# Optimization experiments

Hardware: AMD Instinct MI355X
Metric: run time of the kernel (lower is better)

Reference implementation:

```python
import jax, jax.numpy as jnp
import numpy as np
import math

B, T, D = 2, 2048, 1024
H, HS = 16, 64  # n_heads, head_size; D == H*HS


def setup_inputs() -> dict:
    key = jax.random.key(0)
    k1, k2, k3 = jax.random.split(key, 3)
    x = jax.random.normal(k1, (B, T, D), dtype=jnp.float32)
    w_qkv = jax.random.normal(k2, (D, 3 * D), dtype=jnp.float32) * (1.0 / math.sqrt(D))
    b_qkv = jnp.zeros((3 * D,), dtype=jnp.float32)
    w_out = jax.random.normal(k3, (D, D), dtype=jnp.float32) * (1.0 / math.sqrt(D))
    b_out = jnp.zeros((D,), dtype=jnp.float32)
    return {"x": x, "w_qkv": w_qkv, "b_qkv": b_qkv, "w_out": w_out, "b_out": b_out}


def reference(x, w_qkv, b_qkv, w_out, b_out):
    b, t, d = x.shape
    qkv = x @ w_qkv + b_qkv                       # (B,T,3D)
    q, k, v = jnp.split(qkv, 3, axis=-1)
    # (B,T,D) -> (B,H,T,HS)
    q = q.reshape(b, t, H, HS).transpose(0, 2, 1, 3)
    k = k.reshape(b, t, H, HS).transpose(0, 2, 1, 3)
    v = v.reshape(b, t, H, HS).transpose(0, 2, 1, 3)
    scale = 1.0 / math.sqrt(HS)
    attn = jnp.einsum('bhqd,bhkd->bhqk', q, k) * scale  # (B,H,T,T)
    causal = jnp.tril(jnp.ones((t, t), dtype=bool))
    attn = jnp.where(causal[None, None], attn, -jnp.inf)
    attn = jax.nn.softmax(attn, axis=-1)
    o = jnp.einsum('bhqk,bhkd->bhqd', attn, v)          # (B,H,T,HS)
    o = o.transpose(0, 2, 1, 3).reshape(b, t, d)
    return o @ w_out + b_out
```

## Files before the change

### kernel.cpp

```cpp
#include <hip/hip_runtime.h>
#include <math.h>

#define B_  2
#define T_  2048
#define D_  1024
#define H_  16
#define HS_ 64
#define M_  (B_*T_)

typedef __bf16 bf16x8 __attribute__((ext_vector_type(8)));
typedef float  f32x4  __attribute__((ext_vector_type(4)));
typedef unsigned short u16;

static __device__ __forceinline__ u16 f2bf(float f) {
    __bf16 h = (__bf16)f;
    return *reinterpret_cast<u16*>(&h);
}

static __device__ __forceinline__ void glds16(const u16* g, u16* l) {
    __builtin_amdgcn_global_load_lds(
        (const __attribute__((address_space(1))) void*)g,
        (__attribute__((address_space(3))) void*)l, 16, 0, 0);
}

__global__ __launch_bounds__(256) void prep_kernel(
    const float* __restrict__ x, const float* __restrict__ w_qkv,
    const float* __restrict__ w_out,
    u16* __restrict__ Xb, u16* __restrict__ WqkvT, u16* __restrict__ WoutT)
{
    int bid = blockIdx.x;
    if (bid < 4096) {
        int i = (bid * 256 + threadIdx.x) * 4;
        float4 v = *reinterpret_cast<const float4*>(x + i);
        ushort4 o;
        o.x = f2bf(v.x); o.y = f2bf(v.y); o.z = f2bf(v.z); o.w = f2bf(v.w);
        *reinterpret_cast<ushort4*>(Xb + i) = o;
        return;
    }
    const float* in; u16* out; int C; int c0, r0;
    if (bid < 4096 + 3072) {
        int t = bid - 4096;
        in = w_qkv; out = WqkvT; C = 3 * D_;
        c0 = (t % 96) * 32; r0 = (t / 96) * 32;
    } else {
        int t = bid - 7168;
        in = w_out; out = WoutT; C = D_;
        c0 = (t & 31) * 32; r0 = (t >> 5) * 32;
    }
    __shared__ float tile[32][33];
    int tr = threadIdx.x >> 3, tc4 = (threadIdx.x & 7) * 4;
    float4 v = *reinterpret_cast<const float4*>(in + (size_t)(r0 + tr) * C + c0 + tc4);
    tile[tr][tc4+0] = v.x; tile[tr][tc4+1] = v.y;
    tile[tr][tc4+2] = v.z; tile[tr][tc4+3] = v.w;
    __syncthreads();
    ushort4 o;
    o.x = f2bf(tile[tc4+0][tr]); o.y = f2bf(tile[tc4+1][tr]);
    o.z = f2bf(tile[tc4+2][tr]); o.w = f2bf(tile[tc4+3][tr]);
    *reinterpret_cast<ushort4*>(out + (size_t)(c0 + tr) * D_ + r0 + tc4) = o;
}

__global__ __launch_bounds__(512, 2) void gemm_qkv(
    const u16* __restrict__ A, const u16* __restrict__ Bt,
    const float* __restrict__ bias,
    u16* __restrict__ Qb, u16* __restrict__ Kb, u16* __restrict__ Vt)
{
    constexpr int K  = D_;
    constexpr int NT = K / 64;

    __shared__ u16 LDS[2][2][2][8192];

    const int tid  = threadIdx.x;
    const int lane = tid & 63, wave = tid >> 6;
    const int wm = wave >> 2, wn = wave & 3;
    const int quad = lane >> 4, lr = lane & 15;
    const int bm = blockIdx.x, bn = blockIdx.y;

    const u16* Ab = A  + (size_t)(bm * 256) * K;
    const u16* Bb = Bt + (size_t)(bn * 256) * K;

    const int r0 = tid >> 2;
    const int c0 = (tid & 3) ^ ((tid >> 3) & 3);
    const u16* sA0 = Ab + (size_t)r0 * K + c0 * 8;
    const u16* sA1 = sA0 + (size_t)128 * K;
    const u16* sB0 = Bb + (size_t)r0 * K + c0 * 8;
    const u16* sB1 = sB0 + (size_t)128 * K;
    const int d0 = tid * 8, d1 = (tid + 512) * 8;

    const int swz = (lr >> 1) & 3;
    const int eA = ((wm*128 + lr) * 4 + (quad ^ swz)) * 8;
    const int eB = ((wn*64  + lr) * 4 + (quad ^ swz)) * 8;

    f32x4 acc[8][4] = {};

#define STG(mat, kh, tt) do { \
        u16* _d = &LDS[(tt) & 1][mat][kh][0]; \
        const int _ko = (tt) * 64 + (kh) * 32; \
        glds16(((mat) ? sB0 : sA0) + _ko, _d + d0); \
        glds16(((mat) ? sB1 : sA1) + _ko, _d + d1); \
    } while (0)

#define MFMA_QUAD(mh) do { \
        __builtin_amdgcn_s_setprio(1); \
        _Pragma("unroll") \
        for (int i_ = 0; i_ < 4; ++i_) \
            _Pragma("unroll") \
            for (int j_ = 0; j_ < 4; ++j_) \
                acc[(mh)*4 + i_][j_] = __builtin_amdgcn_mfma_f32_16x16x32_bf16( \
                    a[i_], b[j_], acc[(mh)*4 + i_][j_], 0, 0, 0); \
        __builtin_amdgcn_s_setprio(0); \
    } while (0)

    STG(0,0,0); STG(1,0,0); STG(0,1,0); STG(1,1,0);
    asm volatile("s_waitcnt vmcnt(4)" ::: "memory");
    __builtin_amdgcn_s_barrier();

    for (int t = 0; t < NT; ++t) {
        const int cb = t & 1;
        const bool last = (t == NT - 1);
        const u16* Ar0 = &LDS[cb][0][0][0];
        const u16* Ar1 = &LDS[cb][0][1][0];
        const u16* Br0 = &LDS[cb][1][0][0];
        const u16* Br1 = &LDS[cb][1][1][0];
        bf16x8 a[4], b[4];

        #pragma unroll
        for (int i = 0; i < 4; ++i) a[i] = *reinterpret_cast<const bf16x8*>(Ar0 + eA + i*512);
        #pragma unroll
        for (int j = 0; j < 4; ++j) b[j] = *reinterpret_cast<const bf16x8*>(Br0 + eB + j*512);
        if (!last) STG(0,0,t+1);
        __builtin_amdgcn_s_barrier();
        asm volatile("s_waitcnt lgkmcnt(0)" ::: "memory");
        MFMA_QUAD(0);
        __builtin_amdgcn_s_barrier();

        #pragma unroll
        for (int i = 0; i < 4; ++i) a[i] = *reinterpret_cast<const bf16x8*>(Ar0 + eA + (i+4)*512);
        if (!last) STG(1,0,t+1);
        __builtin_amdgcn_s_barrier();
        asm volatile("s_waitcnt lgkmcnt(0)" ::: "memory");
        MFMA_QUAD(1);
        if (!last) { asm volatile("s_waitcnt vmcnt(4)" ::: "memory"); }
        else       { asm volatile("s_waitcnt vmcnt(0)" ::: "memory"); }
        __builtin_amdgcn_s_barrier();

        #pragma unroll
        for (int i = 0; i < 4; ++i) a[i] = *reinterpret_cast<const bf16x8*>(Ar1 + eA + i*512);
        #pragma unroll
        for (int j = 0; j < 4; ++j) b[j] = *reinterpret_cast<const bf16x8*>(Br1 + eB + j*512);
        if (!last) STG(0,1,t+1);
        __builtin_amdgcn_s_barrier();
        asm volatile("s_waitcnt lgkmcnt(0)" ::: "memory");
        MFMA_QUAD(0);
        __builtin_amdgcn_s_barrier();

        #pragma unroll
        for (int i = 0; i < 4; ++i) a[i] = *reinterpret_cast<const bf16x8*>(Ar1 + eA + (i+4)*512);
        if (!last) STG(1,1,t+1);
        __builtin_amdgcn_s_barrier();
        asm volatile("s_waitcnt lgkmcnt(0)" ::: "memory");
        MFMA_QUAD(1);
        asm volatile("s_waitcnt vmcnt(4)" ::: "memory");
        __builtin_amdgcn_s_barrier();
    }
#undef STG
#undef MFMA_QUAD

    #pragma unroll
    for (int i = 0; i < 8; ++i) {
        int m0 = bm*256 + wm*128 + i*16 + quad*4;
        #pragma unroll
        for (int j = 0; j < 4; ++j) {
            int ncol = bn*256 + wn*64 + j*16 + lr;
            float bv = bias[ncol];
            float v4[4];
            #pragma unroll
            for (int r = 0; r < 4; ++r) v4[r] = acc[i][j][r] + bv;
            int bb = m0 >> 11, t0 = m0 & (T_ - 1);
            int s = ncol >> 10, rem = ncol & 1023;
            int h = rem >> 6, d = rem & 63;
            int bh = bb * H_ + h;
            if (s == 0) {
                #pragma unroll
                for (int r = 0; r < 4; ++r)
                    Qb[((size_t)bh*T_ + t0 + r)*HS_ + d] = f2bf(v4[r] * 0.1803368801111244f);
            } else if (s == 1) {
                #pragma unroll
                for (int r = 0; r < 4; ++r)
                    Kb[((size_t)bh*T_ + t0 + r)*HS_ + d] = f2bf(v4[r]);
            } else {
                ushort4 o;
                o.x = f2bf(v4[0]); o.y = f2bf(v4[1]);
                o.z = f2bf(v4[2]); o.w = f2bf(v4[3]);
                *reinterpret_cast<ushort4*>(&Vt[((size_t)bh*HS_ + d)*T_ + t0]) = o;
            }
        }
    }
}

template<int MODE, int BM, int BN, int WM, int WN, int NTH>
__global__ __launch_bounds__(NTH, 2) void gemm_bt2(
    const u16* __restrict__ A, const u16* __restrict__ Bt,
    const float* __restrict__ bias,
    float* __restrict__ Cf,
    int M, int N, int K)
{
    constexpr int MF  = BM / WM / 16;
    constexpr int NF  = BN / WN / 16;
    constexpr int NLA = BM * 8 / NTH;
    constexpr int NLB = BN * 8 / NTH;

    __shared__ u16 As[2][BM * 64];
    __shared__ u16 Bs[2][BN * 64];

    const int tid  = threadIdx.x;
    const int lane = tid & 63, wave = tid >> 6;
    const int wm = wave / WN, wn = wave % WN;
    const int quad = lane >> 4, lr = lane & 15, x7 = lane & 7;
    const int bm = blockIdx.x, bn = blockIdx.y;

    const u16* Ab = A  + (size_t)(bm * BM) * K;
    const u16* Bb = Bt + (size_t)(bn * BN) * K;

    const u16* srcA[NLA]; int dA[NLA];
    const u16* srcB[NLB]; int dB[NLB];
    #pragma unroll
    for (int j = 0; j < NLA; ++j) {
        int ci = j * NTH + tid, r = ci >> 3, c = (ci & 7) ^ (r & 7);
        srcA[j] = Ab + (size_t)r * K + c * 8;
        dA[j] = ci * 8;
    }
    #pragma unroll
    for (int j = 0; j < NLB; ++j) {
        int ci = j * NTH + tid, r = ci >> 3, c = (ci & 7) ^ (r & 7);
        srcB[j] = Bb + (size_t)r * K + c * 8;
        dB[j] = ci * 8;
    }

    const int eA0 = (wm*(BM/WM) + lr)*64 + ((quad    ) ^ x7)*8;
    const int eA1 = (wm*(BM/WM) + lr)*64 + ((quad | 4) ^ x7)*8;
    const int eB0 = (wn*(BN/WN) + lr)*64 + ((quad    ) ^ x7)*8;
    const int eB1 = (wn*(BN/WN) + lr)*64 + ((quad | 4) ^ x7)*8;

    f32x4 acc[MF][NF] = {};
    const int NT = K >> 6;

    #pragma unroll
    for (int j = 0; j < NLA; ++j) glds16(srcA[j], &As[0][dA[j]]);
    #pragma unroll
    for (int j = 0; j < NLB; ++j) glds16(srcB[j], &Bs[0][dB[j]]);
    #pragma unroll
    for (int j = 0; j < NLA; ++j) glds16(srcA[j] + 64, &As[1][dA[j]]);
    #pragma unroll
    for (int j = 0; j < NLB; ++j) glds16(srcB[j] + 64, &Bs[1][dB[j]]);
    asm volatile("s_waitcnt vmcnt(8)" ::: "memory");
    __builtin_amdgcn_s_barrier();

    for (int t = 0; t < NT; ++t) {
        const u16* Ac = As[t & 1];
        const u16* Bc = Bs[t & 1];
        bf16x8 a[MF], b[NF];

        #pragma unroll
        for (int i = 0; i < MF; ++i)
            a[i] = *reinterpret_cast<const bf16x8*>(Ac + eA0 + i*1024);
        #pragma unroll
        for (int j = 0; j < NF; ++j)
            b[j] = *reinterpret_cast<const bf16x8*>(Bc + eB0 + j*1024);
        __builtin_amdgcn_s_setprio(1);
        #pragma unroll
        for (int i = 0; i < MF; ++i)
            #pragma unroll
            for (int j = 0; j < NF; ++j)
                acc[i][j] = __builtin_amdgcn_mfma_f32_16x16x32_bf16(a[i], b[j], acc[i][j], 0, 0, 0);
        __builtin_amdgcn_s_setprio(0);

        #pragma unroll
        for (int i = 0; i < MF; ++i)
            a[i] = *reinterpret_cast<const bf16x8*>(Ac + eA1 + i*1024);
        #pragma unroll
        for (int j = 0; j < NF; ++j)
            b[j] = *reinterpret_cast<const bf16x8*>(Bc + eB1 + j*1024);
        asm volatile("s_waitcnt lgkmcnt(0)" ::: "memory");
        __builtin_amdgcn_s_barrier();

        if (t + 2 < NT) {
            const int k0 = (t + 2) << 6;
            u16* Ad = As[t & 1]; u16* Bd = Bs[t & 1];
            #pragma unroll
            for (int j = 0; j < NLA; ++j) glds16(srcA[j] + k0, Ad + dA[j]);
            #pragma unroll
            for (int j = 0; j < NLB; ++j) glds16(srcB[j] + k0, Bd + dB[j]);
        }

        __builtin_amdgcn_s_setprio(1);
        #pragma unroll
        for (int i = 0; i < MF; ++i)
            #pragma unroll
            for (int j = 0; j < NF; ++j)
                acc[i][j] = __builtin_amdgcn_mfma_f32_16x16x32_bf16(a[i], b[j], acc[i][j], 0, 0, 0);
        __builtin_amdgcn_s_setprio(0);

        if (t + 2 < NT) { asm volatile("s_waitcnt vmcnt(8)" ::: "memory"); }
        else           { asm volatile("s_waitcnt vmcnt(0)" ::: "memory"); }
        __builtin_amdgcn_s_barrier();
    }

    #pragma unroll
    for (int i = 0; i < MF; ++i) {
        int m0 = bm*BM + wm*(BM/WM) + i*16 + quad*4;
        #pragma unroll
        for (int j = 0; j < NF; ++j) {
            int ncol = bn*BN + wn*(BN/WN) + j*16 + lr;
            float bv = bias[ncol];
            #pragma unroll
            for (int r = 0; r < 4; ++r)
                Cf[(size_t)(m0 + r) * N + ncol] = acc[i][j][r] + bv;
        }
    }
}

__global__ __launch_bounds__(256) void attn_kernel(
    const u16* __restrict__ Qb, const u16* __restrict__ Kb,
    const u16* __restrict__ Vt, u16* __restrict__ Ob)
{
    __shared__ u16 Ks[64 * 64];
    __shared__ u16 Vs[64 * 64];
    __shared__ u16 Ps[4][16 * 64];

    int tid  = threadIdx.x;
    int lane = tid & 63, wave = tid >> 6;
    int quad = lane >> 4, lr = lane & 15;

    int lin = blockIdx.x;
    int bh  = (lin & 7) + 8 * ((lin >> 3) & 3);
    int idx = lin >> 5;
    int qt  = idx < 16 ? idx : 47 - idx;
    int qw  = qt * 64 + wave * 16;

    const u16* Qp = Qb + ((size_t)bh * T_ + qw) * HS_;
    bf16x8 qf[2];
    #pragma unroll
    for (int h2 = 0; h2 < 2; ++h2)
        qf[h2] = *reinterpret_cast<const bf16x8*>(Qp + lr*HS_ + h2*32 + quad*8);

    f32x4 Oa[4] = {};
    float lrow[4] = {0.f, 0.f, 0.f, 0.f};

    int e      = quad ^ (lr & 7);
    int rb0    = (lr * 8 + e) * 8;
    int rb1    = (lr * 8 + (e ^ 4)) * 8;
    int offw[4][4];
    #pragma unroll
    for (int nt = 0; nt < 4; ++nt)
        #pragma unroll
        for (int r = 0; r < 4; ++r) {
            int prow = quad*4 + r;
            offw[nt][r] = (prow*8 + ((nt*2 + (lr >> 3)) ^ (prow & 7)))*8 + (lr & 7);
        }
    u16* Psw = Ps[wave];

    int srow = tid >> 3;
    int scol = ((tid & 7) ^ (srow & 7)) * 8;
    const u16* kp0 = Kb + ((size_t)bh*T_ + srow     )*HS_ + scol;
    const u16* kp1 = Kb + ((size_t)bh*T_ + srow + 32)*HS_ + scol;
    const u16* vp0 = Vt + ((size_t)bh*HS_ + srow     )*T_ + scol;
    const u16* vp1 = Vt + ((size_t)bh*HS_ + srow + 32)*T_ + scol;

    bf16x8 kpre0 = *reinterpret_cast<const bf16x8*>(kp0);
    bf16x8 kpre1 = *reinterpret_cast<const bf16x8*>(kp1);
    bf16x8 vpre0 = *reinterpret_cast<const bf16x8*>(vp0);
    bf16x8 vpre1 = *reinterpret_cast<const bf16x8*>(vp1);

    for (int jt = 0; jt <= qt; ++jt) {
        __syncthreads();
        reinterpret_cast<bf16x8*>(Ks)[tid]       = kpre0;
        reinterpret_cast<bf16x8*>(Ks)[tid + 256] = kpre1;
        reinterpret_cast<bf16x8*>(Vs)[tid]       = vpre0;
        reinterpret_cast<bf16x8*>(Vs)[tid + 256] = vpre1;
        if (jt < qt) {
            kp0 += 64*HS_; kp1 += 64*HS_; vp0 += 64; vp1 += 64;
            kpre0 = *reinterpret_cast<const bf16x8*>(kp0);
            kpre1 = *reinterpret_cast<const bf16x8*>(kp1);
            vpre0 = *reinterpret_cast<const bf16x8*>(vp0);
            vpre1 = *reinterpret_cast<const bf16x8*>(vp1);
        }
        __syncthreads();

        f32x4 Sa[4] = {};
        #pragma unroll
        for (int nt = 0; nt < 4; ++nt) {
            bf16x8 bk0 = *reinterpret_cast<const bf16x8*>(Ks + rb0 + nt*1024);
            bf16x8 bk1 = *reinterpret_cast<const bf16x8*>(Ks + rb1 + nt*1024);
            Sa[nt] = __builtin_amdgcn_mfma_f32_16x16x32_bf16(qf[0], bk0, Sa[nt], 0, 0, 0);
            Sa[nt] = __builtin_amdgcn_mfma_f32_16x16x32_bf16(qf[1], bk1, Sa[nt], 0, 0, 0);
        }

        if (jt == qt) {
            int kb = jt * 64;
            #pragma unroll
            for (int nt = 0; nt < 4; ++nt)
                #pragma unroll
                for (int r = 0; r < 4; ++r) {
                    int kg = kb + nt*16 + lr;
                    int qg = qw + quad*4 + r;
                    if (kg > qg) Sa[nt][r] = -INFINITY;
                }
        }

        #pragma unroll
        for (int nt = 0; nt < 4; ++nt)
            #pragma unroll
            for (int r = 0; r < 4; ++r) {
                float pv = __builtin_amdgcn_exp2f(Sa[nt][r]);
                lrow[r] += pv;
                Psw[offw[nt][r]] = f2bf(pv);
            }

        #pragma unroll
        for (int kk = 0; kk < 2; ++kk) {
            int rb = kk ? rb1 : rb0;
            bf16x8 pa = *reinterpret_cast<const bf16x8*>(Psw + rb);
            #pragma unroll
            for (int nt = 0; nt < 4; ++nt) {
                bf16x8 vb = *reinterpret_cast<const bf16x8*>(Vs + rb + nt*1024);
                Oa[nt] = __builtin_amdgcn_mfma_f32_16x16x32_bf16(pa, vb, Oa[nt], 0, 0, 0);
            }
        }
    }

    int b = bh >> 4, h = bh & 15;
    #pragma unroll
    for (int r = 0; r < 4; ++r) {
        float s = lrow[r];
        #pragma unroll
        for (int off = 8; off >= 1; off >>= 1)
            s += __shfl_xor(s, off, 64);
        float inv = 1.f / s;
        int qg = qw + quad*4 + r;
        #pragma unroll
        for (int nt = 0; nt < 4; ++nt) {
            int d = nt*16 + lr;
            Ob[((size_t)b*T_ + qg)*D_ + h*HS_ + d] = f2bf(Oa[nt][r] * inv);
        }
    }
}

extern "C" void kernel_launch(void* const* d_in, const int* in_sizes, int n_in,
                              void* d_out, int out_size, void* d_ws, size_t ws_size,
                              hipStream_t stream) {
    (void)in_sizes; (void)n_in; (void)out_size; (void)ws_size;
    const float* x     = (const float*)d_in[0];
    const float* w_qkv = (const float*)d_in[1];
    const float* b_qkv = (const float*)d_in[2];
    const float* w_out = (const float*)d_in[3];
    const float* b_out = (const float*)d_in[4];
    float* out = (float*)d_out;

    char* ws = (char*)d_ws;
    u16* Xb    = (u16*)ws; ws += (size_t)M_ * D_ * 2;
    u16* WqkvT = (u16*)ws; ws += (size_t)3 * D_ * D_ * 2;
    u16* WoutT = (u16*)ws; ws += (size_t)D_ * D_ * 2;
    u16* Qb    = (u16*)ws; ws += (size_t)M_ * D_ * 2;
    u16* Kb    = (u16*)ws; ws += (size_t)M_ * D_ * 2;
    u16* Vt    = (u16*)ws; ws += (size_t)M_ * D_ * 2;
    u16* Ob    = (u16*)ws; ws += (size_t)M_ * D_ * 2;

    prep_kernel<<<8192, 256, 0, stream>>>(x, w_qkv, w_out, Xb, WqkvT, WoutT);
    gemm_qkv<<<dim3(M_/256, 3*D_/256), 512, 0, stream>>>(
        Xb, WqkvT, b_qkv, Qb, Kb, Vt);
    attn_kernel<<<1024, 256, 0, stream>>>(Qb, Kb, Vt, Ob);
    gemm_bt2<1, 128, 128, 2, 2, 256><<<dim3(M_/128, D_/128), 256, 0, stream>>>(
        Ob, WoutT, b_out, out, M_, D_, D_);
}
```

Baseline: 174.1 us.

## Rewrite output GEMM with half-K-step LDS staging and finer prefetch

Replaces the templated output-projection GEMM with a specialized 128x128 kernel. Each 64-wide K tile is split into two 32-wide halves in separate LDS buffers with a new 4-way XOR swizzle, and the next tile's half is prefetched right after the current half's fragments are read. The aim is finer-grained overlap of global-to-LDS loads with MFMA work and keeping the prefetch only one tile ahead. The cost is more barriers per K step, and the shallower prefetch depth (one tile ahead instead of two) may expose more memory latency.

```diff
diff --git a/kernel.cpp b/kernel.cpp
--- a/kernel.cpp
+++ b/kernel.cpp
@@ -197,120 +197,107 @@
     }
 }
 
-template<int MODE, int BM, int BN, int WM, int WN, int NTH>
-__global__ __launch_bounds__(NTH, 2) void gemm_bt2(
+__global__ __launch_bounds__(256, 2) void gemm_out(
     const u16* __restrict__ A, const u16* __restrict__ Bt,
-    const float* __restrict__ bias,
-    float* __restrict__ Cf,
-    int M, int N, int K)
+    const float* __restrict__ bias, float* __restrict__ Cf)
 {
-    constexpr int MF  = BM / WM / 16;
-    constexpr int NF  = BN / WN / 16;
-    constexpr int NLA = BM * 8 / NTH;
-    constexpr int NLB = BN * 8 / NTH;
-
-    __shared__ u16 As[2][BM * 64];
-    __shared__ u16 Bs[2][BN * 64];
+    constexpr int K  = D_;
+    constexpr int N  = D_;
+    constexpr int NT = K / 64;
+
+    __shared__ u16 LDS[2][2][2][4096];
 
     const int tid  = threadIdx.x;
     const int lane = tid & 63, wave = tid >> 6;
-    const int wm = wave / WN, wn = wave % WN;
-    const int quad = lane >> 4, lr = lane & 15, x7 = lane & 7;
+    const int wm = wave >> 1, wn = wave & 1;
+    const int quad = lane >> 4, lr = lane & 15;
     const int bm = blockIdx.x, bn = blockIdx.y;
 
-    const u16* Ab = A  + (size_t)(bm * BM) * K;
-    const u16* Bb = Bt + (size_t)(bn * BN) * K;
-
-    const u16* srcA[NLA]; int dA[NLA];
-    const u16* srcB[NLB]; int dB[NLB];
+    const u16* Ab = A  + (size_t)(bm * 128) * K;
+    const u16* Bb = Bt + (size_t)(bn * 128) * K;
+
+    const int r0 = tid >> 2;
+    const int c0 = (tid & 3) ^ ((tid >> 3) & 3);
+    const u16* sA0 = Ab + (size_t)r0 * K + c0 * 8;
+    const u16* sA1 = sA0 + (size_t)64 * K;
+    const u16* sB0 = Bb + (size_t)r0 * K + c0 * 8;
+    const u16* sB1 = sB0 + (size_t)64 * K;
+    const int d0 = tid * 8, d1 = (tid + 256) * 8;
+
+    const int swz = (lr >> 1) & 3;
+    const int eA = ((wm*64 + lr) * 4 + (quad ^ swz)) * 8;
+    const int eB = ((wn*64 + lr) * 4 + (quad ^ swz)) * 8;
+
+    f32x4 acc[4][4] = {};
+
+#define STGO(kh, tt) do { \
+        const int _ko = (tt) * 64 + (kh) * 32; \
+        glds16(sA0 + _ko, &LDS[(tt) & 1][0][kh][0] + d0); \
+        glds16(sA1 + _ko, &LDS[(tt) & 1][0][kh][0] + d1); \
+        glds16(sB0 + _ko, &LDS[(tt) & 1][1][kh][0] + d0); \
+        glds16(sB1 + _ko, &LDS[(tt) & 1][1][kh][0] + d1); \
+    } while (0)
+
+    STGO(0, 0); STGO(1, 0);
+    asm volatile("s_waitcnt vmcnt(4)" ::: "memory");
+    __builtin_amdgcn_s_barrier();
+
+    for (int t = 0; t < NT; ++t) {
+        const int cb = t & 1;
+        const bool last = (t == NT - 1);
+        bf16x8 a[4], b[4];
+
+        {
+            const u16* Ar = &LDS[cb][0][0][0];
+            const u16* Br = &LDS[cb][1][0][0];
+            #pragma unroll
+            for (int i = 0; i < 4; ++i) a[i] = *reinterpret_cast<const bf16x8*>(Ar + eA + i*512);
+            #pragma unroll
+            for (int j = 0; j < 4; ++j) b[j] = *reinterpret_cast<const bf16x8*>(Br + eB + j*512);
+            if (!last) STGO(0, t+1);
+            __builtin_amdgcn_s_barrier();
+            asm volatile("s_waitcnt lgkmcnt(0)" ::: "memory");
+            __builtin_amdgcn_s_setprio(1);
+            #pragma unroll
+            for (int i = 0; i < 4; ++i)
+                #pragma unroll
+                for (int j = 0; j < 4; ++j)
+                    acc[i][j] = __builtin_amdgcn_mfma_f32_16x16x32_bf16(a[i], b[j], acc[i][j], 0, 0, 0);
+            __builtin_amdgcn_s_setprio(0);
+            if (!last) { asm volatile("s_waitcnt vmcnt(4)" ::: "memory"); }
+            else       { asm volatile("s_waitcnt vmcnt(0)" ::: "memory"); }
+            __builtin_amdgcn_s_barrier();
+        }
+
+        {
+            const u16* Ar = &LDS[cb][0][1][0];
+            const u16* Br = &LDS[cb][1][1][0];
+            #pragma unroll
+            for (int i = 0; i < 4; ++i) a[i] = *reinterpret_cast<const bf16x8*>(Ar + eA + i*512);
+            #pragma unroll
+            for (int j = 0; j < 4; ++j) b[j] = *reinterpret_cast<const bf16x8*>(Br + eB + j*512);
+            if (!last) STGO(1, t+1);
+            __builtin_amdgcn_s_barrier();
+            asm volatile("s_waitcnt lgkmcnt(0)" ::: "memory");
+            __builtin_amdgcn_s_setprio(1);
+            #pragma unroll
+            for (int i = 0; i < 4; ++i)
+                #pragma unroll
+                for (int j = 0; j < 4; ++j)
+                    acc[i][j] = __builtin_amdgcn_mfma_f32_16x16x32_bf16(a[i], b[j], acc[i][j], 0, 0, 0);
+            __builtin_amdgcn_s_setprio(0);
+            if (!last) { asm volatile("s_waitcnt vmcnt(4)" ::: "memory"); }
+            __builtin_amdgcn_s_barrier();
+        }
+    }
+#undef STGO
+
     #pragma unroll
-    for (int j = 0; j < NLA; ++j) {
-        int ci = j * NTH + tid, r = ci >> 3, c = (ci & 7) ^ (r & 7);
-        srcA[j] = Ab + (size_t)r * K + c * 8;
-        dA[j] = ci * 8;
-    }
-    #pragma unroll
-    for (int j = 0; j < NLB; ++j) {
-        int ci = j * NTH + tid, r = ci >> 3, c = (ci & 7) ^ (r & 7);
-        srcB[j] = Bb + (size_t)r * K + c * 8;
-        dB[j] = ci * 8;
-    }
-
-    const int eA0 = (wm*(BM/WM) + lr)*64 + ((quad    ) ^ x7)*8;
-    const int eA1 = (wm*(BM/WM) + lr)*64 + ((quad | 4) ^ x7)*8;
-    const int eB0 = (wn*(BN/WN) + lr)*64 + ((quad    ) ^ x7)*8;
-    const int eB1 = (wn*(BN/WN) + lr)*64 + ((quad | 4) ^ x7)*8;
-
-    f32x4 acc[MF][NF] = {};
-    const int NT = K >> 6;
-
-    #pragma unroll
-    for (int j = 0; j < NLA; ++j) glds16(srcA[j], &As[0][dA[j]]);
-    #pragma unroll
-    for (int j = 0; j < NLB; ++j) glds16(srcB[j], &Bs[0][dB[j]]);
-    #pragma unroll
-    for (int j = 0; j < NLA; ++j) glds16(srcA[j] + 64, &As[1][dA[j]]);
-    #pragma unroll
-    for (int j = 0; j < NLB; ++j) glds16(srcB[j] + 64, &Bs[1][dB[j]]);
-    asm volatile("s_waitcnt vmcnt(8)" ::: "memory");
-    __builtin_amdgcn_s_barrier();
-
-    for (int t = 0; t < NT; ++t) {
-        const u16* Ac = As[t & 1];
-        const u16* Bc = Bs[t & 1];
-        bf16x8 a[MF], b[NF];
-
-        #pragma unroll
-        for (int i = 0; i < MF; ++i)
-            a[i] = *reinterpret_cast<const bf16x8*>(Ac + eA0 + i*1024);
-        #pragma unroll
-        for (int j = 0; j < NF; ++j)
-            b[j] = *reinterpret_cast<const bf16x8*>(Bc + eB0 + j*1024);
-        __builtin_amdgcn_s_setprio(1);
-        #pragma unroll
-        for (int i = 0; i < MF; ++i)
-            #pragma unroll
-            for (int j = 0; j < NF; ++j)
-                acc[i][j] = __builtin_amdgcn_mfma_f32_16x16x32_bf16(a[i], b[j], acc[i][j], 0, 0, 0);
-        __builtin_amdgcn_s_setprio(0);
-
-        #pragma unroll
-        for (int i = 0; i < MF; ++i)
-            a[i] = *reinterpret_cast<const bf16x8*>(Ac + eA1 + i*1024);
-        #pragma unroll
-        for (int j = 0; j < NF; ++j)
-            b[j] = *reinterpret_cast<const bf16x8*>(Bc + eB1 + j*1024);
-        asm volatile("s_waitcnt lgkmcnt(0)" ::: "memory");
-        __builtin_amdgcn_s_barrier();
-
-        if (t + 2 < NT) {
-            const int k0 = (t + 2) << 6;
-            u16* Ad = As[t & 1]; u16* Bd = Bs[t & 1];
-            #pragma unroll
-            for (int j = 0; j < NLA; ++j) glds16(srcA[j] + k0, Ad + dA[j]);
-            #pragma unroll
-            for (int j = 0; j < NLB; ++j) glds16(srcB[j] + k0, Bd + dB[j]);
-        }
-
-        __builtin_amdgcn_s_setprio(1);
-        #pragma unroll
-        for (int i = 0; i < MF; ++i)
-            #pragma unroll
-            for (int j = 0; j < NF; ++j)
-                acc[i][j] = __builtin_amdgcn_mfma_f32_16x16x32_bf16(a[i], b[j], acc[i][j], 0, 0, 0);
-        __builtin_amdgcn_s_setprio(0);
-
-        if (t + 2 < NT) { asm volatile("s_waitcnt vmcnt(8)" ::: "memory"); }
-        else           { asm volatile("s_waitcnt vmcnt(0)" ::: "memory"); }
-        __builtin_amdgcn_s_barrier();
-    }
-
-    #pragma unroll
-    for (int i = 0; i < MF; ++i) {
-        int m0 = bm*BM + wm*(BM/WM) + i*16 + quad*4;
-        #pragma unroll
-        for (int j = 0; j < NF; ++j) {
-            int ncol = bn*BN + wn*(BN/WN) + j*16 + lr;
+    for (int i = 0; i < 4; ++i) {
+        int m0 = bm*128 + wm*64 + i*16 + quad*4;
+        #pragma unroll
+        for (int j = 0; j < 4; ++j) {
+            int ncol = bn*128 + wn*64 + j*16 + lr;
             float bv = bias[ncol];
             #pragma unroll
             for (int r = 0; r < 4; ++r)
@@ -469,6 +456,5 @@
     gemm_qkv<<<dim3(M_/256, 3*D_/256), 512, 0, stream>>>(
         Xb, WqkvT, b_qkv, Qb, Kb, Vt);
     attn_kernel<<<1024, 256, 0, stream>>>(Qb, Kb, Vt, Ob);
-    gemm_bt2<1, 128, 128, 2, 2, 256><<<dim3(M_/128, D_/128), 256, 0, stream>>>(
-        Ob, WoutT, b_out, out, M_, D_, D_);
-}
+    gemm_out<<<dim3(M_/128, D_/128), 256, 0, stream>>>(Ob, WoutT, b_out, out);
+}
```

Measured after the change: 171.7 us (median of 2 runs). No clear change (-1.4%).
